# Kernel optimization log

Measured on AMD Instinct MI355X. Metric: run time of the kernel, lower is better.

Reference implementation:

```python
import jax, jax.numpy as jnp
import numpy as np

IN_DIM = 128
OUT_DIM = 128
NUM_HEADS = 4
HEAD_DIM = OUT_DIM // NUM_HEADS
TEMP = 0.2
NEG_SLOPE = 0.2


def _xavier(key, shape, gain=1.414):
    fan_in, fan_out = shape[-2], shape[-1]
    limit = gain * np.sqrt(6.0 / (fan_in + fan_out))
    return jax.random.uniform(key, shape, jnp.float32, -limit, limit)


def setup_inputs() -> dict:
    key = jax.random.key(0)
    k_h, k_W, k_a, k_mw, k_mb = jax.random.split(key, 5)
    B, N = 4, 2048
    h = jax.random.normal(k_h, (B, N, IN_DIM), jnp.float32)
    W = _xavier(k_W, (NUM_HEADS, IN_DIM, HEAD_DIM))
    a = _xavier(k_a, (NUM_HEADS, 2 * HEAD_DIM, 1))
    merge_w = _xavier(k_mw, (OUT_DIM, OUT_DIM))  # nn.Linear weight [out, in]
    merge_b = jnp.zeros((OUT_DIM,), jnp.float32)
    return {"h": h, "W": W, "a": a, "merge_w": merge_w, "merge_b": merge_b}


def reference(h, W, a, merge_w, merge_b):
    B, N, _ = h.shape
    # Wh: [B, H, N, head_dim]
    Wh = jnp.einsum('bni,hio->bhno', h, W)
    a_sq = a[..., 0]                                  # [H, 2*hd]
    a_src, a_dst = a_sq[:, :HEAD_DIM], a_sq[:, HEAD_DIM:]
    # additive score decomposition avoids the NxNx2hd concat blowup
    s_src = jnp.einsum('bhno,ho->bhn', Wh, a_src)     # contribution of node i (row)
    s_dst = jnp.einsum('bhno,ho->bhn', Wh, a_dst)     # contribution of node j (col)
    e = s_src[:, :, :, None] + s_dst[:, :, None, :]   # [B, H, N, N]
    e = jnp.where(e > 0, e, NEG_SLOPE * e)            # LeakyReLU(0.2)
    alpha = jax.nn.softmax(e / TEMP, axis=3)          # softmax over neighbors j
    h_prime_heads = jnp.einsum('bhnm,bhmo->bhno', alpha, Wh)
    h_concat = h_prime_heads.transpose(0, 2, 1, 3).reshape(B, N, OUT_DIM)
    h_prime = h_concat @ merge_w.T + merge_b
    return h_prime, alpha.mean(axis=1)
```

## Files before the change

### kernel.cpp

```cpp
#include <hip/hip_runtime.h>
#include <stddef.h>

#define NN 2048
#define DIN 128
#define HD 32

typedef __attribute__((ext_vector_type(8))) short short8;
typedef __attribute__((ext_vector_type(4))) float f32x4;
typedef __attribute__((ext_vector_type(4))) unsigned short us4;

constexpr float SLOPE = 0.2f;
constexpr float LC = 7.2134752044448170f;

__device__ __forceinline__ unsigned int pack_rne(float a, float b){
    unsigned int xa = __float_as_uint(a), xb = __float_as_uint(b);
    unsigned int ra = (xa + 0x7fffu + ((xa >> 16) & 1u)) >> 16;
    unsigned int rb = (xb + 0x7fffu + ((xb >> 16) & 1u)) >> 16;
    return ra | (rb << 16);
}

__device__ __forceinline__ unsigned short bf16_rne(float a){
    unsigned int x = __float_as_uint(a);
    return (unsigned short)((x + 0x7fffu + ((x >> 16) & 1u)) >> 16);
}

__device__ __forceinline__ float fexp2(float x){
    float r; asm("v_exp_f32 %0, %1" : "=v"(r) : "v"(x)); return r;
}

__global__ __launch_bounds__(256) void kPrep(const float* __restrict__ Wg,
                                             const float* __restrict__ mw,
                                             unsigned short* __restrict__ BtHi,
                                             unsigned short* __restrict__ BtLo,
                                             unsigned short* __restrict__ mwB)
{
    const int t = threadIdx.x;
    if (blockIdx.x < 16){
        const int col = blockIdx.x*8 + (t>>5);
        const int i0  = (t&31)*4;
        const int h = col >> 5, o = col & 31;
        us4 vh, vl;
        #pragma unroll
        for (int j = 0; j < 4; ++j){
            const float w = Wg[(h*DIN + i0 + j)*HD + o];
            const unsigned short hi = bf16_rne(w);
            const float hf = __uint_as_float((unsigned int)hi << 16);
            vh[j] = hi;
            vl[j] = bf16_rne(w - hf);
        }
        *(us4*)&BtHi[col*DIN + i0] = vh;
        *(us4*)&BtLo[col*DIN + i0] = vl;
    } else {
        const int col = (blockIdx.x - 16)*8 + (t>>5);
        const int k0  = (t&31)*4;
        const f32x4 v = *(const f32x4*)&mw[col*128 + k0];
        us4 p;
        #pragma unroll
        for (int j = 0; j < 4; ++j) p[j] = bf16_rne(v[j]);
        *(us4*)&mwB[col*128 + k0] = p;
    }
}

__global__ __launch_bounds__(256) void kWh(const float* __restrict__ hg,
                                           const unsigned short* __restrict__ BtHi,
                                           const unsigned short* __restrict__ BtLo,
                                           const float* __restrict__ ag,
                                           unsigned short* __restrict__ WhT,
                                           float* __restrict__ sSrc,
                                           float* __restrict__ sDst,
                                           float* __restrict__ maxPartW)
{
    __shared__ float Hl[16][DIN+4];
    const int t = threadIdx.x;
    const int wv = t >> 6, lane = t & 63;
    const int q = lane >> 4, c = lane & 15;
    const int r0 = blockIdx.x * 16;
    const int b  = r0 >> 11;
    const int n0 = r0 & (NN-1);
    {
        const int r = t >> 5, c4 = t & 31;
        *(float4*)&Hl[r][c4*4] = *(const float4*)&hg[((size_t)b*NN + n0 + r)*DIN + c4*4];
        const int f2 = t + 256, r2 = f2 >> 5, c42 = f2 & 31;
        *(float4*)&Hl[r2][c42*4] = *(const float4*)&hg[((size_t)b*NN + n0 + r2)*DIN + c42*4];
    }
    __syncthreads();
    short8 Ahi[4], Alo[4];
    #pragma unroll
    for (int k = 0; k < 4; ++k){
        const float* sp = &Hl[c][k*32 + q*8];
        #pragma unroll
        for (int j2 = 0; j2 < 2; ++j2){
            const f32x4 x = *(const f32x4*)&sp[j2*4];
            #pragma unroll
            for (int j = 0; j < 4; ++j){
                const unsigned short hi = bf16_rne(x[j]);
                const float hf = __uint_as_float((unsigned int)hi << 16);
                ((unsigned short*)&Ahi[k])[j2*4+j] = hi;
                ((unsigned short*)&Alo[k])[j2*4+j] = bf16_rne(x[j] - hf);
            }
        }
    }
    const int hh = wv;
    const int bh = b*4 + hh;
    f32x4 acc0 = {0.f,0.f,0.f,0.f}, acc1 = {0.f,0.f,0.f,0.f};
    #pragma unroll
    for (int k = 0; k < 4; ++k){
        const int koff = k*32 + q*8;
        const short8 Bh0 = *(const short8*)&BtHi[(hh*32      + c)*DIN + koff];
        const short8 Bl0 = *(const short8*)&BtLo[(hh*32      + c)*DIN + koff];
        const short8 Bh1 = *(const short8*)&BtHi[(hh*32 + 16 + c)*DIN + koff];
        const short8 Bl1 = *(const short8*)&BtLo[(hh*32 + 16 + c)*DIN + koff];
        acc0 = __builtin_amdgcn_mfma_f32_16x16x32_bf16(Ahi[k], Bh0, acc0, 0, 0, 0);
        acc1 = __builtin_amdgcn_mfma_f32_16x16x32_bf16(Ahi[k], Bh1, acc1, 0, 0, 0);
        acc0 = __builtin_amdgcn_mfma_f32_16x16x32_bf16(Ahi[k], Bl0, acc0, 0, 0, 0);
        acc1 = __builtin_amdgcn_mfma_f32_16x16x32_bf16(Ahi[k], Bl1, acc1, 0, 0, 0);
        acc0 = __builtin_amdgcn_mfma_f32_16x16x32_bf16(Alo[k], Bh0, acc0, 0, 0, 0);
        acc1 = __builtin_amdgcn_mfma_f32_16x16x32_bf16(Alo[k], Bh1, acc1, 0, 0, 0);
    }
    {
        us4 w0, w1;
        #pragma unroll
        for (int reg = 0; reg < 4; ++reg){
            w0[reg] = bf16_rne(acc0[reg]);
            w1[reg] = bf16_rne(acc1[reg]);
        }
        *(us4*)&WhT[((size_t)bh*32      + c)*NN + n0 + q*4] = w0;
        *(us4*)&WhT[((size_t)bh*32 + 16 + c)*NN + n0 + q*4] = w1;
    }
    const float aS0 = ag[hh*64 + c],      aS1 = ag[hh*64 + 16 + c];
    const float aD0 = ag[hh*64 + 32 + c], aD1 = ag[hh*64 + 48 + c];
    float vs[4], vd[4];
    #pragma unroll
    for (int reg = 0; reg < 4; ++reg){
        vs[reg] = acc0[reg]*aS0 + acc1[reg]*aS1;
        vd[reg] = acc0[reg]*aD0 + acc1[reg]*aD1;
    }
    #pragma unroll
    for (int m = 1; m <= 8; m <<= 1){
        #pragma unroll
        for (int reg = 0; reg < 4; ++reg){
            vs[reg] += __shfl_xor(vs[reg], m);
            vd[reg] += __shfl_xor(vd[reg], m);
        }
    }
    if (c == 0){
        *(f32x4*)&sSrc[(size_t)bh*NN + n0 + q*4] = (f32x4){vs[0],vs[1],vs[2],vs[3]};
        *(f32x4*)&sDst[(size_t)bh*NN + n0 + q*4] = (f32x4){vd[0],vd[1],vd[2],vd[3]};
    }
    float wm = fmaxf(fmaxf(vd[0],vd[1]), fmaxf(vd[2],vd[3]));
    wm = fmaxf(wm, __shfl_xor(wm, 16));
    wm = fmaxf(wm, __shfl_xor(wm, 32));
    if (lane == 0) maxPartW[bh*128 + (n0 >> 4)] = wm;
}

__global__ __launch_bounds__(256) void kAttnM(const unsigned short* __restrict__ WhT,
                                              const float* __restrict__ sSrc,
                                              const float* __restrict__ sDst,
                                              const float* __restrict__ maxPartW,
                                              float* __restrict__ invZ,
                                              unsigned short* __restrict__ hcb)
{
    __shared__ float sdl[NN];
    __shared__ float smax[4];
    const int t = threadIdx.x;
    const int lane = t & 63;
    const int wv = t >> 6;
    const int q = lane >> 4, c = lane & 15;
    const int bh = blockIdx.x >> 5;
    const int n0 = (blockIdx.x & 31)*64 + wv*16;
    const int b = bh >> 2, hh = bh & 3;
    for (int i = t; i < NN; i += 256) sdl[i] = LC * sDst[bh*NN + i];
    {
        float v = maxPartW[bh*128 + ((wv&1)<<6) + lane];
        #pragma unroll
        for (int off = 32; off; off >>= 1) v = fmaxf(v, __shfl_xor(v, off));
        if (lane == 0) smax[wv] = v;
    }
    const float ssrc = sSrc[bh*NN + n0 + c];
    __syncthreads();
    const float mx = fmaxf(fmaxf(smax[0], smax[1]), fmaxf(smax[2], smax[3]));
    const float q0v = ssrc + mx;
    const float R = fmaxf(q0v, SLOPE*q0v) * LC;
    const float a1 = ssrc*LC - R;
    const float a2 = SLOPE*LC*ssrc - R;
    const unsigned short* wb0 = WhT + (size_t)bh*32*NN + (size_t)c*NN + q*8;
    const unsigned short* wb1 = wb0 + (size_t)16*NN;
    f32x4 acc0 = {0.f,0.f,0.f,0.f}, acc1 = {0.f,0.f,0.f,0.f};
    float Zp = 0.f;
    short8 bF0 = *(const short8*)&wb0[0];
    short8 bF1 = *(const short8*)&wb1[0];
    #pragma unroll 4
    for (int it = 0; it < 64; ++it){
        const int m8 = it*32 + q*8;
        const int nx = ((it+1) & 63)*32;
        const short8 nF0 = *(const short8*)&wb0[nx];
        const short8 nF1 = *(const short8*)&wb1[nx];
        const f32x4 u0 = *(const f32x4*)&sdl[m8];
        const f32x4 u1 = *(const f32x4*)&sdl[m8+4];
        float p[8];
        #pragma unroll
        for (int j = 0; j < 4; ++j){
            p[j]   = fexp2(fmaxf(a1 + u0[j], fmaf(SLOPE, u0[j], a2)));
            p[4+j] = fexp2(fmaxf(a1 + u1[j], fmaf(SLOPE, u1[j], a2)));
        }
        short8 aF;
        #pragma unroll
        for (int j = 0; j < 8; j += 2){
            ((unsigned int*)&aF)[j>>1] = (__float_as_uint(p[j]) >> 16)
                                       | (__float_as_uint(p[j+1]) & 0xffff0000u);
            Zp += p[j] + p[j+1];
        }
        acc0 = __builtin_amdgcn_mfma_f32_16x16x32_bf16(aF, bF0, acc0, 0, 0, 0);
        acc1 = __builtin_amdgcn_mfma_f32_16x16x32_bf16(aF, bF1, acc1, 0, 0, 0);
        bF0 = nF0; bF1 = nF1;
    }
    Zp += __shfl_xor(Zp, 16);
    Zp += __shfl_xor(Zp, 32);
    const float iz = 1.0f / Zp;
    if (q == 0) invZ[bh*NN + n0 + c] = iz;
    #pragma unroll
    for (int reg = 0; reg < 4; ++reg){
        const int row = q*4 + reg;
        const float izr = __shfl(iz, row);
        const size_t base = ((size_t)b*NN + n0 + row)*128 + hh*32;
        hcb[base + c]      = (unsigned short)((pack_rne(acc0[reg]*izr, 0.f)) & 0xffffu);
        hcb[base + 16 + c] = (unsigned short)((pack_rne(acc1[reg]*izr, 0.f)) & 0xffffu);
    }
}

__global__ __launch_bounds__(256) void kTail(const float* __restrict__ sSrc,
                                             const float* __restrict__ sDst,
                                             const float* __restrict__ maxPartW,
                                             const float* __restrict__ invZ,
                                             const unsigned short* __restrict__ hcb,
                                             const unsigned short* __restrict__ mwB,
                                             const float* __restrict__ mbv,
                                             float* __restrict__ out0,
                                             float* __restrict__ out1)
{
    __shared__ float sdl[4][NN];
    __shared__ float mxl[4];
    const int t = threadIdx.x;
    const int wv = t >> 6, lane = t & 63;
    if (blockIdx.x < 256){
        const int q = lane >> 4, c = lane & 15;
        const int r0 = blockIdx.x*32 + (wv&1)*16;
        const int ch = (wv>>1)*64;
        f32x4 acc[4];
        #pragma unroll
        for (int ot = 0; ot < 4; ++ot) acc[ot] = (f32x4){0.f,0.f,0.f,0.f};
        #pragma unroll
        for (int ks = 0; ks < 4; ++ks){
            const short8 aF = *(const short8*)&hcb[((size_t)r0 + c)*128 + ks*32 + q*8];
            #pragma unroll
            for (int ot = 0; ot < 4; ++ot){
                const short8 bF = *(const short8*)&mwB[(size_t)(ch + ot*16 + c)*128 + ks*32 + q*8];
                acc[ot] = __builtin_amdgcn_mfma_f32_16x16x32_bf16(aF, bF, acc[ot], 0, 0, 0);
            }
        }
        #pragma unroll
        for (int ot = 0; ot < 4; ++ot){
            const int col = ch + ot*16 + c;
            const float bias = mbv[col];
            #pragma unroll
            for (int reg = 0; reg < 4; ++reg){
                const size_t row = (size_t)r0 + q*4 + reg;
                out0[row*128 + col] = acc[ot][reg] + bias;
            }
        }
        return;
    }
    const int bidA = blockIdx.x - 256;
    const int b = bidA >> 9;
    const int n0 = (bidA & 511) * 4;
    {
        float v = fmaxf(maxPartW[(b*4+wv)*128 + lane], maxPartW[(b*4+wv)*128 + 64 + lane]);
        #pragma unroll
        for (int off = 32; off; off >>= 1) v = fmaxf(v, __shfl_xor(v, off));
        if (lane == 0) mxl[wv] = v;
    }
    for (int i = t; i < 4*NN; i += 256)
        sdl[i >> 11][i & (NN-1)] = LC * sDst[(size_t)(b*4 + (i>>11))*NN + (i & (NN-1))];
    __syncthreads();
    float a1[4][4], a2[4][4], cf[4][4];
    #pragma unroll
    for (int hh = 0; hh < 4; ++hh){
        const float mx = mxl[hh];
        #pragma unroll
        for (int rr = 0; rr < 4; ++rr){
            const int bhn = (b*4+hh)*NN + n0 + rr;
            const float ss = sSrc[bhn];
            const float q0 = ss + mx;
            const float R = fmaxf(q0, SLOPE*q0)*LC;
            a1[rr][hh] = ss*LC - R;
            a2[rr][hh] = SLOPE*LC*ss - R;
            cf[rr][hh] = 0.25f * invZ[bhn];
        }
    }
    for (int mb = 0; mb < NN; mb += 256){
        const int m = mb + t;
        const float u0 = sdl[0][m], u1 = sdl[1][m], u2 = sdl[2][m], u3 = sdl[3][m];
        #pragma unroll
        for (int rr = 0; rr < 4; ++rr){
            float v;
            v  = cf[rr][0]*fexp2(fmaxf(a1[rr][0]+u0, fmaf(SLOPE, u0, a2[rr][0])));
            v += cf[rr][1]*fexp2(fmaxf(a1[rr][1]+u1, fmaf(SLOPE, u1, a2[rr][1])));
            v += cf[rr][2]*fexp2(fmaxf(a1[rr][2]+u2, fmaf(SLOPE, u2, a2[rr][2])));
            v += cf[rr][3]*fexp2(fmaxf(a1[rr][3]+u3, fmaf(SLOPE, u3, a2[rr][3])));
            __builtin_nontemporal_store(v, &out1[((size_t)b*NN + n0 + rr)*NN + m]);
        }
    }
}

extern "C" void kernel_launch(void* const* d_in, const int* in_sizes, int n_in,
                              void* d_out, int out_size, void* d_ws, size_t ws_size,
                              hipStream_t stream)
{
    const float* hg  = (const float*)d_in[0];
    const float* Wg  = (const float*)d_in[1];
    const float* ag  = (const float*)d_in[2];
    const float* mw  = (const float*)d_in[3];
    const float* mbv = (const float*)d_in[4];
    float* out0 = (float*)d_out;
    float* out1 = out0 + (size_t)4*NN*128;

    float* ws      = (float*)d_ws;
    float* sSrc    = ws;
    float* sDst    = sSrc + 32768;
    float* maxPartW= sDst + 32768;
    float* invZ    = maxPartW + 2048;
    unsigned short* hcb  = (unsigned short*)(invZ + 32768);
    unsigned short* WhT  = hcb + 1048576;
    unsigned short* BtHi = WhT + 1048576;
    unsigned short* BtLo = BtHi + 16384;
    unsigned short* mwB  = BtLo + 16384;

    hipLaunchKernelGGL(kPrep,  dim3(32),   dim3(256), 0, stream, Wg, mw, BtHi, BtLo, mwB);
    hipLaunchKernelGGL(kWh,    dim3(512),  dim3(256), 0, stream, hg, BtHi, BtLo, ag, WhT, sSrc, sDst, maxPartW);
    hipLaunchKernelGGL(kAttnM, dim3(512),  dim3(256), 0, stream, WhT, sSrc, sDst, maxPartW, invZ, hcb);
    hipLaunchKernelGGL(kTail,  dim3(2304), dim3(256), 0, stream, sSrc, sDst, maxPartW, invZ, hcb, mwB, mbv, out0, out1);
}
```

Before: 141.5 us.

## Split attention key range across wave pairs with shared-memory reduction

The attention kernel now assigns 32 query rows per block instead of 64. Each 16-row group is handled by two waves that each cover half of the 2048 keys. Partial accumulators and normalizer sums are combined through shared memory before normalizing and storing. The grid doubles to 1024 blocks, which raises parallelism and shortens each wave's serial loop, at the cost of an extra barrier, more shared memory, and twice as many blocks loading the full sDst row into shared memory.

```diff
diff --git a/kernel.cpp b/kernel.cpp
--- a/kernel.cpp
+++ b/kernel.cpp
@@ -162,16 +162,19 @@
 {
     __shared__ float sdl[NN];
     __shared__ float smax[4];
+    __shared__ float red[2][64][9];
     const int t = threadIdx.x;
     const int lane = t & 63;
     const int wv = t >> 6;
     const int q = lane >> 4, c = lane & 15;
-    const int bh = blockIdx.x >> 5;
-    const int n0 = (blockIdx.x & 31)*64 + wv*16;
+    const int bh = blockIdx.x >> 6;
+    const int tile = blockIdx.x & 63;
+    const int rg = wv >> 1, mh = wv & 1;
+    const int n0 = tile*32 + rg*16;
     const int b = bh >> 2, hh = bh & 3;
     for (int i = t; i < NN; i += 256) sdl[i] = LC * sDst[bh*NN + i];
     {
-        float v = maxPartW[bh*128 + ((wv&1)<<6) + lane];
+        float v = maxPartW[bh*128 + (mh<<6) + lane];
         #pragma unroll
         for (int off = 32; off; off >>= 1) v = fmaxf(v, __shfl_xor(v, off));
         if (lane == 0) smax[wv] = v;
@@ -183,20 +186,21 @@
     const float R = fmaxf(q0v, SLOPE*q0v) * LC;
     const float a1 = ssrc*LC - R;
     const float a2 = SLOPE*LC*ssrc - R;
-    const unsigned short* wb0 = WhT + (size_t)bh*32*NN + (size_t)c*NN + q*8;
+    const unsigned short* wb0 = WhT + (size_t)bh*32*NN + (size_t)c*NN + mh*1024 + q*8;
     const unsigned short* wb1 = wb0 + (size_t)16*NN;
+    const float* sdb = &sdl[mh*1024];
     f32x4 acc0 = {0.f,0.f,0.f,0.f}, acc1 = {0.f,0.f,0.f,0.f};
     float Zp = 0.f;
     short8 bF0 = *(const short8*)&wb0[0];
     short8 bF1 = *(const short8*)&wb1[0];
     #pragma unroll 4
-    for (int it = 0; it < 64; ++it){
+    for (int it = 0; it < 32; ++it){
         const int m8 = it*32 + q*8;
-        const int nx = ((it+1) & 63)*32;
+        const int nx = ((it+1) & 31)*32;
         const short8 nF0 = *(const short8*)&wb0[nx];
         const short8 nF1 = *(const short8*)&wb1[nx];
-        const f32x4 u0 = *(const f32x4*)&sdl[m8];
-        const f32x4 u1 = *(const f32x4*)&sdl[m8+4];
+        const f32x4 u0 = *(const f32x4*)&sdb[m8];
+        const f32x4 u1 = *(const f32x4*)&sdb[m8+4];
         float p[8];
         #pragma unroll
         for (int j = 0; j < 4; ++j){
@@ -216,15 +220,32 @@
     }
     Zp += __shfl_xor(Zp, 16);
     Zp += __shfl_xor(Zp, 32);
-    const float iz = 1.0f / Zp;
-    if (q == 0) invZ[bh*NN + n0 + c] = iz;
-    #pragma unroll
-    for (int reg = 0; reg < 4; ++reg){
-        const int row = q*4 + reg;
-        const float izr = __shfl(iz, row);
-        const size_t base = ((size_t)b*NN + n0 + row)*128 + hh*32;
-        hcb[base + c]      = (unsigned short)((pack_rne(acc0[reg]*izr, 0.f)) & 0xffffu);
-        hcb[base + 16 + c] = (unsigned short)((pack_rne(acc1[reg]*izr, 0.f)) & 0xffffu);
+    if (mh == 1){
+        #pragma unroll
+        for (int k2 = 0; k2 < 4; ++k2){
+            red[rg][lane][k2]     = acc0[k2];
+            red[rg][lane][4 + k2] = acc1[k2];
+        }
+        red[rg][lane][8] = Zp;
+    }
+    __syncthreads();
+    if (mh == 0){
+        #pragma unroll
+        for (int k2 = 0; k2 < 4; ++k2){
+            acc0[k2] += red[rg][lane][k2];
+            acc1[k2] += red[rg][lane][4 + k2];
+        }
+        Zp += red[rg][lane][8];
+        const float iz = 1.0f / Zp;
+        if (q == 0) invZ[bh*NN + n0 + c] = iz;
+        #pragma unroll
+        for (int reg = 0; reg < 4; ++reg){
+            const int row = q*4 + reg;
+            const float izr = __shfl(iz, row);
+            const size_t base = ((size_t)b*NN + n0 + row)*128 + hh*32;
+            hcb[base + c]      = (unsigned short)((pack_rne(acc0[reg]*izr, 0.f)) & 0xffffu);
+            hcb[base + 16 + c] = (unsigned short)((pack_rne(acc1[reg]*izr, 0.f)) & 0xffffu);
+        }
     }
 }
 
@@ -337,6 +358,6 @@
 
     hipLaunchKernelGGL(kPrep,  dim3(32),   dim3(256), 0, stream, Wg, mw, BtHi, BtLo, mwB);
     hipLaunchKernelGGL(kWh,    dim3(512),  dim3(256), 0, stream, hg, BtHi, BtLo, ag, WhT, sSrc, sDst, maxPartW);
-    hipLaunchKernelGGL(kAttnM, dim3(512),  dim3(256), 0, stream, WhT, sSrc, sDst, maxPartW, invZ, hcb);
+    hipLaunchKernelGGL(kAttnM, dim3(1024), dim3(256), 0, stream, WhT, sSrc, sDst, maxPartW, invZ, hcb);
     hipLaunchKernelGGL(kTail,  dim3(2304), dim3(256), 0, stream, sSrc, sDst, maxPartW, invZ, hcb, mwB, mbv, out0, out1);
 }
```

After: 140.0 us. No clear change (-1.0%).
